# Optimization experiments

Measured on AMD Instinct MI355X. Metric: run time of the kernel, lower is better.

## Reference

```python
import jax, jax.numpy as jnp
import numpy as np

S, D, P, R, E, M, K = 1024, 1024, 2816, 64, 8, 16, 1


def setup_inputs() -> dict:
    key = jax.random.key(0)
    ks = jax.random.split(key, 10)
    xav_a = (2.0 / (P + R)) ** 0.5   # xavier_uniform-like std for adapters
    xav_d = (2.0 / (D + P)) ** 0.5   # xavier for down projections
    bank_s = (1.0 / D) ** 0.5        # keep basis columns O(1)
    return {
        "hidden_states": jax.random.normal(ks[0], (S, D), jnp.float32),
        "expert_indices": jax.random.randint(ks[1], (S, K), 0, E),
        "expert_weights": jax.random.uniform(ks[2], (S, K), jnp.float32),
        "up_adapters": jax.random.normal(ks[3], (E, P, R), jnp.float32) * xav_a,
        "gate_adapters": jax.random.normal(ks[4], (E, P, R), jnp.float32) * xav_a,
        "up_mixture_logits": jax.random.normal(ks[5], (E, M), jnp.float32) * 0.01,
        "gate_mixture_logits": jax.random.normal(ks[6], (E, M), jnp.float32) * 0.01,
        "down_projections": jax.random.normal(ks[7], (E, D, P), jnp.float32) * xav_d,
        "up_bank": jax.random.normal(ks[8], (M, D, R), jnp.float32) * bank_s,
        "gate_bank": jax.random.normal(ks[9], (M, D, R), jnp.float32) * bank_s,
    }


def reference(hidden_states, expert_indices, expert_weights,
              up_adapters, gate_adapters, up_mixture_logits,
              gate_mixture_logits, down_projections, up_bank, gate_bank):
    n_experts = down_projections.shape[0]
    # SparseMixer: token-independent mixture weights over global bases (softmax)
    alpha_up = jax.nn.softmax(up_mixture_logits, axis=-1)      # [E, M]
    alpha_gate = jax.nn.softmax(gate_mixture_logits, axis=-1)  # [E, M]
    # Compose per-expert mixed bases: sum_j alpha_{e,j} B_j -> [E, D, R]
    up_mixed = jnp.einsum('em,mdr->edr', alpha_up, up_bank)
    gate_mixed = jnp.einsum('em,mdr->edr', alpha_gate, gate_bank)
    # Recomposed Up/Gate weights: A_e @ mixed_e^T -> [E, P, D]
    W_up = jnp.einsum('epr,edr->epd', up_adapters, up_mixed)
    W_gate = jnp.einsum('epr,edr->epd', gate_adapters, gate_mixed)
    # Combine routing weights per (token, expert): sum over topk slots
    onehot = (expert_indices[..., None] == jnp.arange(n_experts)).astype(hidden_states.dtype)  # [S,K,E]
    comb = jnp.einsum('ske,sk->se', onehot, expert_weights)  # [S, E]
    out = jnp.zeros_like(hidden_states)
    for e in range(n_experts):  # fixed small expert count
        up = hidden_states @ W_up[e].T        # [S, P]
        gate = hidden_states @ W_gate[e].T    # [S, P]
        inter = jax.nn.silu(gate) * up        # gated activation
        out = out + (inter @ down_projections[e].T) * comb[:, e:e + 1]
    return out
```

## Files before the change

kernel.cpp:

```cpp
#include <hip/hip_runtime.h>
#include <hip/hip_bf16.h>
#include <math.h>

#define S 1024
#define D 1024
#define P 2816
#define R 64
#define E 8
#define M 16
#define KSPLIT 4
#define KQ (P / KSPLIT)
#define NIT (KQ / 64)
#define ZT 8
#define ACH ((E * P * R) / 8)

typedef __attribute__((ext_vector_type(8))) short short8;
typedef __attribute__((ext_vector_type(4))) float floatx4;

static __device__ inline unsigned short f2bf(float f) {
  __hip_bfloat16 h = __float2bfloat16(f);
  return *reinterpret_cast<unsigned short*>(&h);
}
static __device__ inline short8 pack8(float4 a, float4 b) {
  short8 v;
  v[0] = f2bf(a.x); v[1] = f2bf(a.y); v[2] = f2bf(a.z); v[3] = f2bf(a.w);
  v[4] = f2bf(b.x); v[5] = f2bf(b.y); v[6] = f2bf(b.z); v[7] = f2bf(b.w);
  return v;
}

__global__ __launch_bounds__(256) void k_pre(
    const float* __restrict__ up_logits, const float* __restrict__ gate_logits,
    const float* __restrict__ up_bank, const float* __restrict__ gate_bank,
    const float* __restrict__ H, const float* __restrict__ Aup,
    const float* __restrict__ Agate, const int* __restrict__ idx,
    unsigned short* __restrict__ Hbf, unsigned short* __restrict__ mxT,
    unsigned short* __restrict__ Aubf, unsigned short* __restrict__ Agbf,
    int* __restrict__ perm, int* __restrict__ offs) {
  int b = blockIdx.x, t = threadIdx.x;
  int g = b * 256 + t;

  if (b == 0) {
    __shared__ int hist[E];
    __shared__ int basearr[E];
    if (t < E) hist[t] = 0;
    __syncthreads();
    int e4[4];
#pragma unroll
    for (int j = 0; j < 4; ++j) {
      e4[j] = idx[t + j * 256];
      atomicAdd(&hist[e4[j]], 1);
    }
    __syncthreads();
    if (t == 0) {
      int run = 0;
      for (int i = 0; i < E; ++i) { basearr[i] = run; offs[i] = run; run += hist[i]; }
      offs[E] = S;
    }
    __syncthreads();
#pragma unroll
    for (int j = 0; j < 4; ++j) {
      int pos = atomicAdd(&basearr[e4[j]], 1);
      perm[pos] = t + j * 256;
    }
  }

  {
    const float* hs = H + (size_t)g * 16;
    float4 h0 = *(const float4*)hs, h1 = *(const float4*)(hs + 4);
    float4 h2 = *(const float4*)(hs + 8), h3 = *(const float4*)(hs + 12);
    *(short8*)(Hbf + (size_t)g * 16) = pack8(h0, h1);
    *(short8*)(Hbf + (size_t)g * 16 + 8) = pack8(h2, h3);
  }
#pragma unroll
  for (int j = 0; j < 3; ++j) {
    int c = g + j * 65536;
    if (c < ACH) {
      const float* su = Aup + (size_t)c * 8;
      const float* sg = Agate + (size_t)c * 8;
      float4 u0 = *(const float4*)su, u1 = *(const float4*)(su + 4);
      float4 g0 = *(const float4*)sg, g1 = *(const float4*)(sg + 4);
      *(short8*)(Aubf + (size_t)c * 8) = pack8(u0, u1);
      *(short8*)(Agbf + (size_t)c * 8) = pack8(g0, g1);
    }
  }

  __shared__ float alpha[2][E][M];
  if (t < 16) {
    int mat = t >> 3, e = t & 7;
    const float* lg = (mat ? gate_logits : up_logits) + e * M;
    float v[M], mx = -1e30f, s = 0.f;
#pragma unroll
    for (int m = 0; m < M; ++m) { v[m] = lg[m]; mx = fmaxf(mx, v[m]); }
#pragma unroll
    for (int m = 0; m < M; ++m) { v[m] = expf(v[m] - mx); s += v[m]; }
#pragma unroll
    for (int m = 0; m < M; ++m) alpha[mat][e][m] = v[m] / s;
  }
  __syncthreads();
  int d = g >> 6, r = g & 63;
  float au[E] = {0, 0, 0, 0, 0, 0, 0, 0}, ag[E] = {0, 0, 0, 0, 0, 0, 0, 0};
#pragma unroll
  for (int m = 0; m < M; ++m) {
    float vu = up_bank[((size_t)m * D + d) * R + r];
    float vg = gate_bank[((size_t)m * D + d) * R + r];
#pragma unroll
    for (int e = 0; e < E; ++e) {
      au[e] += alpha[0][e][m] * vu;
      ag[e] += alpha[1][e][m] * vg;
    }
  }
#pragma unroll
  for (int e = 0; e < E; ++e) {
    mxT[((size_t)e * 128 + r) * D + d] = f2bf(au[e]);
    mxT[((size_t)e * 128 + 64 + r) * D + d] = f2bf(ag[e]);
  }
}

__global__ __launch_bounds__(64) void k_t(
    const unsigned short* __restrict__ Hbf, const unsigned short* __restrict__ mxT,
    const int* __restrict__ perm, const int* __restrict__ offs,
    float* __restrict__ tpart) {
  int e = blockIdx.x;
  int end = offs[e + 1];
  int row0 = offs[e] + blockIdx.y * 16;
  if (row0 >= end) return;
  int lane = threadIdx.x & 63;
  int quad = lane >> 4, l15 = lane & 15;
  int z = blockIdx.z;
  int k0 = z * (D / ZT);
  int pos = row0 + l15;
  int tok = (pos < end) ? perm[pos] : -1;
  const unsigned short* hrow = Hbf + (size_t)(tok < 0 ? 0 : tok) * D + k0;
  const unsigned short* brow = mxT + (size_t)e * 128 * D + k0;
  floatx4 acc[8];
#pragma unroll
  for (int nt = 0; nt < 8; ++nt) acc[nt] = (floatx4){0.f, 0.f, 0.f, 0.f};
#pragma unroll
  for (int ks = 0; ks < 4; ++ks) {
    int kc = ks * 32 + quad * 8;
    short8 a = (short8){0, 0, 0, 0, 0, 0, 0, 0};
    if (tok >= 0) a = *(const short8*)(hrow + kc);
#pragma unroll
    for (int nt = 0; nt < 8; ++nt) {
      short8 bb = *(const short8*)(brow + (size_t)(nt * 16 + l15) * D + kc);
      acc[nt] = __builtin_amdgcn_mfma_f32_16x16x32_bf16(a, bb, acc[nt], 0, 0, 0);
    }
  }
#pragma unroll
  for (int reg = 0; reg < 4; ++reg) {
    int p = row0 + quad * 4 + reg;
    if (p < end) {
#pragma unroll
      for (int nt = 0; nt < 8; ++nt)
        tpart[((size_t)z * S + p) * 128 + nt * 16 + l15] = acc[nt][reg];
    }
  }
}

__global__ __launch_bounds__(256) void k_tred(
    const float* __restrict__ tpart, unsigned short* __restrict__ tbuf) {
  int i = (blockIdx.x * 256 + threadIdx.x) * 2;
  float2 s = make_float2(0.f, 0.f);
#pragma unroll
  for (int z = 0; z < ZT; ++z) {
    float2 v = *(const float2*)(tpart + (size_t)z * S * 128 + i);
    s.x += v.x; s.y += v.y;
  }
  unsigned int pk = (unsigned int)f2bf(s.x) | ((unsigned int)f2bf(s.y) << 16);
  *(unsigned int*)(tbuf + i) = pk;
}

__global__ __launch_bounds__(256) void k_inter(
    const unsigned short* __restrict__ tbuf, const unsigned short* __restrict__ Aubf,
    const unsigned short* __restrict__ Agbf, const int* __restrict__ offs,
    unsigned short* __restrict__ inter) {
  int e = blockIdx.x;
  int start = offs[e] + blockIdx.y * 16;
  int end = offs[e + 1];
  if (start >= end) return;
  int t = threadIdx.x, lane = t & 63, w = t >> 6;
  int quad = lane >> 4, l15 = lane & 15;
  int p0 = blockIdx.z * 256 + w * 64;
  int pos = start + l15;
  bool okA = pos < end;
  floatx4 accu[4], accg[4];
#pragma unroll
  for (int nt = 0; nt < 4; ++nt) {
    accu[nt] = (floatx4){0.f, 0.f, 0.f, 0.f};
    accg[nt] = (floatx4){0.f, 0.f, 0.f, 0.f};
  }
#pragma unroll
  for (int ks = 0; ks < 2; ++ks) {
    int kc = ks * 32 + quad * 8;
    short8 au = (short8){0, 0, 0, 0, 0, 0, 0, 0};
    short8 ag = (short8){0, 0, 0, 0, 0, 0, 0, 0};
    if (okA) {
      au = *(const short8*)(tbuf + (size_t)pos * 128 + kc);
      ag = *(const short8*)(tbuf + (size_t)pos * 128 + 64 + kc);
    }
#pragma unroll
    for (int nt = 0; nt < 4; ++nt) {
      size_t prow = (size_t)e * P + p0 + nt * 16 + l15;
      short8 bu = *(const short8*)(Aubf + prow * R + kc);
      short8 bg = *(const short8*)(Agbf + prow * R + kc);
      accu[nt] = __builtin_amdgcn_mfma_f32_16x16x32_bf16(au, bu, accu[nt], 0, 0, 0);
      accg[nt] = __builtin_amdgcn_mfma_f32_16x16x32_bf16(ag, bg, accg[nt], 0, 0, 0);
    }
  }
#pragma unroll
  for (int nt = 0; nt < 4; ++nt)
#pragma unroll
    for (int reg = 0; reg < 4; ++reg) {
      int prow = start + quad * 4 + reg;
      if (prow < end) {
        float gv = accg[nt][reg], uv = accu[nt][reg];
        float val = uv * (gv / (1.f + __expf(-gv)));
        inter[(size_t)prow * P + p0 + nt * 16 + l15] = f2bf(val);
      }
    }
}

__global__ __launch_bounds__(256) void k_down(
    const unsigned short* __restrict__ inter, const float* __restrict__ Wd,
    const int* __restrict__ offs, float* __restrict__ dpart) {
  int e = blockIdx.x;
  int start = offs[e];
  int end = offs[e + 1];
  if (start >= end) return;
  int kz = blockIdx.y;
  int d0 = blockIdx.z * 64;
  __shared__ unsigned short As[256][72];
  __shared__ unsigned short Bs[64][72];
  int t = threadIdx.x;
  int lane = t & 63, w = t >> 6, quad = lane >> 4, l15 = lane & 15;

  const unsigned short* aptr[8];
  bool aok[8];
#pragma unroll
  for (int j = 0; j < 8; ++j) {
    int arow = (t >> 3) + 32 * j;
    int pos = start + arow;
    aok[j] = (pos < end);
    aptr[j] = inter + (size_t)(aok[j] ? pos : start) * P + kz * KQ + (t & 7) * 8;
  }
  const float* bsrc = Wd + ((size_t)(e * D + d0 + (t >> 2)) * P + kz * KQ + (t & 3) * 16);

  float4 pa[8];
  float4 pb[4];
#pragma unroll
  for (int j = 0; j < 8; ++j)
    pa[j] = aok[j] ? *(const float4*)(aptr[j]) : make_float4(0.f, 0.f, 0.f, 0.f);
#pragma unroll
  for (int q = 0; q < 4; ++q) pb[q] = *(const float4*)(bsrc + q * 4);

  floatx4 acc[4][4];
#pragma unroll
  for (int tt = 0; tt < 4; ++tt)
#pragma unroll
    for (int dt = 0; dt < 4; ++dt) acc[tt][dt] = (floatx4){0.f, 0.f, 0.f, 0.f};

  for (int it = 0; it < NIT; ++it) {
#pragma unroll
    for (int j = 0; j < 8; ++j)
      *(float4*)&As[(t >> 3) + 32 * j][(t & 7) * 8] = pa[j];
    {
      short8 bv0, bv1;
      bv0[0] = f2bf(pb[0].x); bv0[1] = f2bf(pb[0].y); bv0[2] = f2bf(pb[0].z); bv0[3] = f2bf(pb[0].w);
      bv0[4] = f2bf(pb[1].x); bv0[5] = f2bf(pb[1].y); bv0[6] = f2bf(pb[1].z); bv0[7] = f2bf(pb[1].w);
      bv1[0] = f2bf(pb[2].x); bv1[1] = f2bf(pb[2].y); bv1[2] = f2bf(pb[2].z); bv1[3] = f2bf(pb[2].w);
      bv1[4] = f2bf(pb[3].x); bv1[5] = f2bf(pb[3].y); bv1[6] = f2bf(pb[3].z); bv1[7] = f2bf(pb[3].w);
      *(short8*)&Bs[t >> 2][(t & 3) * 16] = bv0;
      *(short8*)&Bs[t >> 2][(t & 3) * 16 + 8] = bv1;
    }
    __syncthreads();
    if (it + 1 < NIT) {
      int k0 = (it + 1) * 64;
#pragma unroll
      for (int j = 0; j < 8; ++j)
        pa[j] = aok[j] ? *(const float4*)(aptr[j] + k0) : make_float4(0.f, 0.f, 0.f, 0.f);
#pragma unroll
      for (int q = 0; q < 4; ++q) pb[q] = *(const float4*)(bsrc + k0 + q * 4);
    }
#pragma unroll
    for (int ks = 0; ks < 2; ++ks) {
      int kc = ks * 32 + quad * 8;
      short8 a[4], b[4];
#pragma unroll
      for (int tt = 0; tt < 4; ++tt) a[tt] = *(const short8*)&As[w * 64 + tt * 16 + l15][kc];
#pragma unroll
      for (int dt = 0; dt < 4; ++dt) b[dt] = *(const short8*)&Bs[dt * 16 + l15][kc];
#pragma unroll
      for (int tt = 0; tt < 4; ++tt)
#pragma unroll
        for (int dt = 0; dt < 4; ++dt)
          acc[tt][dt] = __builtin_amdgcn_mfma_f32_16x16x32_bf16(a[tt], b[dt], acc[tt][dt], 0, 0, 0);
    }
    __syncthreads();
  }
  float* dp = dpart + (size_t)kz * S * D;
#pragma unroll
  for (int tt = 0; tt < 4; ++tt)
#pragma unroll
    for (int reg = 0; reg < 4; ++reg) {
      int pos = start + w * 64 + tt * 16 + quad * 4 + reg;
      if (pos < end) {
#pragma unroll
        for (int dt = 0; dt < 4; ++dt)
          dp[(size_t)pos * D + d0 + dt * 16 + l15] = acc[tt][dt][reg];
      }
    }
}

__global__ __launch_bounds__(256) void k_red(
    const float* __restrict__ dpart, const int* __restrict__ perm,
    const float* __restrict__ wts, float* __restrict__ out) {
  int t = threadIdx.x;
  int row = blockIdx.x * 4 + (t >> 6);
  int lane = t & 63;
  int tok = perm[row];
  float wt = wts[tok];
  const float* src = dpart + (size_t)row * D + lane * 4;
  float* dst = out + (size_t)tok * D + lane * 4;
#pragma unroll
  for (int j = 0; j < 4; ++j) {
    float4 s = *(const float4*)(src + j * 256);
#pragma unroll
    for (int kz = 1; kz < KSPLIT; ++kz) {
      float4 v = *(const float4*)(src + (size_t)kz * S * D + j * 256);
      s.x += v.x; s.y += v.y; s.z += v.z; s.w += v.w;
    }
    s.x *= wt; s.y *= wt; s.z *= wt; s.w *= wt;
    *(float4*)(dst + j * 256) = s;
  }
}

extern "C" void kernel_launch(void* const* d_in, const int* in_sizes, int n_in,
                              void* d_out, int out_size, void* d_ws, size_t ws_size,
                              hipStream_t stream) {
  const float* H = (const float*)d_in[0];
  const int* idx = (const int*)d_in[1];
  const float* wts = (const float*)d_in[2];
  const float* Aup = (const float*)d_in[3];
  const float* Agate = (const float*)d_in[4];
  const float* upl = (const float*)d_in[5];
  const float* gatel = (const float*)d_in[6];
  const float* Wd = (const float*)d_in[7];
  const float* upb = (const float*)d_in[8];
  const float* gateb = (const float*)d_in[9];
  float* out = (float*)d_out;

  char* ws = (char*)d_ws;
  unsigned short* Hbf = (unsigned short*)ws;
  unsigned short* mxT = Hbf + (size_t)S * D;
  unsigned short* Aubf = mxT + (size_t)E * 128 * D;
  unsigned short* Agbf = Aubf + (size_t)E * P * R;
  unsigned short* inter = Agbf + (size_t)E * P * R;
  unsigned short* tbuf = inter + (size_t)S * P;
  float* tpart = (float*)(tbuf + (size_t)S * 128);
  float* dpart = tpart + (size_t)ZT * S * 128;
  int* perm = (int*)(dpart + (size_t)KSPLIT * S * D);
  int* offs = perm + S;

  k_pre<<<256, 256, 0, stream>>>(upl, gatel, upb, gateb, H, Aup, Agate, idx,
                                 Hbf, mxT, Aubf, Agbf, perm, offs);
  k_t<<<dim3(E, 16, ZT), 64, 0, stream>>>(Hbf, mxT, perm, offs, tpart);
  k_tred<<<256, 256, 0, stream>>>(tpart, tbuf);
  k_inter<<<dim3(E, 16, P / 256), 256, 0, stream>>>(tbuf, Aubf, Agbf, offs, inter);
  k_down<<<dim3(E, KSPLIT, D / 64), 256, 0, stream>>>(inter, Wd, offs, dpart);
  k_red<<<256, 256, 0, stream>>>(dpart, perm, wts, out);
}
```

Before: 217.6 us.

## Split basis mixing into tiled kernel with coalesced transposed stores; double k_t split-K

The softmax-weighted basis mixing moves out of k_pre into a new k_mix kernel. It reads the banks as float4, transposes through an LDS tile, and writes mxT in contiguous 16-element bf16 chunks instead of scattered 2-byte stores strided by D. Separately, the k_t split-K factor goes from 8 to 16 with half the inner k-steps, giving more blocks for the small token-by-basis GEMM. The cost is one extra kernel launch and a larger partial buffer for k_tred to reduce.

```diff
diff --git a/kernel.cpp b/kernel.cpp
--- a/kernel.cpp
+++ b/kernel.cpp
@@ -11,7 +11,7 @@
 #define KSPLIT 4
 #define KQ (P / KSPLIT)
 #define NIT (KQ / 64)
-#define ZT 8
+#define ZT 16
 #define ACH ((E * P * R) / 8)
 
 typedef __attribute__((ext_vector_type(8))) short short8;
@@ -29,13 +29,11 @@
 }
 
 __global__ __launch_bounds__(256) void k_pre(
-    const float* __restrict__ up_logits, const float* __restrict__ gate_logits,
-    const float* __restrict__ up_bank, const float* __restrict__ gate_bank,
     const float* __restrict__ H, const float* __restrict__ Aup,
     const float* __restrict__ Agate, const int* __restrict__ idx,
-    unsigned short* __restrict__ Hbf, unsigned short* __restrict__ mxT,
-    unsigned short* __restrict__ Aubf, unsigned short* __restrict__ Agbf,
-    int* __restrict__ perm, int* __restrict__ offs) {
+    unsigned short* __restrict__ Hbf, unsigned short* __restrict__ Aubf,
+    unsigned short* __restrict__ Agbf, int* __restrict__ perm,
+    int* __restrict__ offs) {
   int b = blockIdx.x, t = threadIdx.x;
   int g = b * 256 + t;
 
@@ -83,36 +81,63 @@
       *(short8*)(Agbf + (size_t)c * 8) = pack8(g0, g1);
     }
   }
-
-  __shared__ float alpha[2][E][M];
-  if (t < 16) {
-    int mat = t >> 3, e = t & 7;
-    const float* lg = (mat ? gate_logits : up_logits) + e * M;
+}
+
+__global__ __launch_bounds__(256) void k_mix(
+    const float* __restrict__ up_logits, const float* __restrict__ gate_logits,
+    const float* __restrict__ up_bank, const float* __restrict__ gate_bank,
+    unsigned short* __restrict__ mxT) {
+  int mat = blockIdx.x;
+  int d0 = blockIdx.y * 16;
+  const float* bank = mat ? gate_bank : up_bank;
+  __shared__ float alpha[E][M];
+  __shared__ float tile[E][64][17];
+  int t = threadIdx.x;
+  if (t < E) {
+    const float* lg = (mat ? gate_logits : up_logits) + t * M;
     float v[M], mx = -1e30f, s = 0.f;
 #pragma unroll
     for (int m = 0; m < M; ++m) { v[m] = lg[m]; mx = fmaxf(mx, v[m]); }
 #pragma unroll
     for (int m = 0; m < M; ++m) { v[m] = expf(v[m] - mx); s += v[m]; }
 #pragma unroll
-    for (int m = 0; m < M; ++m) alpha[mat][e][m] = v[m] / s;
+    for (int m = 0; m < M; ++m) alpha[t][m] = v[m] / s;
   }
   __syncthreads();
-  int d = g >> 6, r = g & 63;
-  float au[E] = {0, 0, 0, 0, 0, 0, 0, 0}, ag[E] = {0, 0, 0, 0, 0, 0, 0, 0};
-#pragma unroll
+  int r4 = (t & 15) * 4;
+  int dg = t >> 4;
+  float val[E][4];
+#pragma unroll
+  for (int e = 0; e < E; ++e)
+#pragma unroll
+    for (int i = 0; i < 4; ++i) val[e][i] = 0.f;
   for (int m = 0; m < M; ++m) {
-    float vu = up_bank[((size_t)m * D + d) * R + r];
-    float vg = gate_bank[((size_t)m * D + d) * R + r];
+    float4 bv = *(const float4*)(bank + ((size_t)m * D + d0 + dg) * R + r4);
 #pragma unroll
     for (int e = 0; e < E; ++e) {
-      au[e] += alpha[0][e][m] * vu;
-      ag[e] += alpha[1][e][m] * vg;
-    }
-  }
-#pragma unroll
-  for (int e = 0; e < E; ++e) {
-    mxT[((size_t)e * 128 + r) * D + d] = f2bf(au[e]);
-    mxT[((size_t)e * 128 + 64 + r) * D + d] = f2bf(ag[e]);
+      float a = alpha[e][m];
+      val[e][0] += a * bv.x; val[e][1] += a * bv.y;
+      val[e][2] += a * bv.z; val[e][3] += a * bv.w;
+    }
+  }
+#pragma unroll
+  for (int e = 0; e < E; ++e)
+#pragma unroll
+    for (int i = 0; i < 4; ++i) tile[e][r4 + i][dg] = val[e][i];
+  __syncthreads();
+  int e = t >> 5;
+#pragma unroll
+  for (int half = 0; half < 2; ++half) {
+    int rr = (t & 31) + half * 32;
+    short8 o0, o1;
+#pragma unroll
+    for (int j = 0; j < 8; ++j) {
+      o0[j] = (short)f2bf(tile[e][rr][j]);
+      o1[j] = (short)f2bf(tile[e][rr][8 + j]);
+    }
+    unsigned short* dst = mxT + ((size_t)(e * 128 + mat * 64 + rr)) * D + d0;
+    *(short8*)dst = o0;
+    *(short8*)(dst + 8) = o1;
   }
 }
 
@@ -136,7 +161,7 @@
 #pragma unroll
   for (int nt = 0; nt < 8; ++nt) acc[nt] = (floatx4){0.f, 0.f, 0.f, 0.f};
 #pragma unroll
-  for (int ks = 0; ks < 4; ++ks) {
+  for (int ks = 0; ks < 2; ++ks) {
     int kc = ks * 32 + quad * 8;
     short8 a = (short8){0, 0, 0, 0, 0, 0, 0, 0};
     if (tok >= 0) a = *(const short8*)(hrow + kc);
@@ -361,8 +386,8 @@
   int* perm = (int*)(dpart + (size_t)KSPLIT * S * D);
   int* offs = perm + S;
 
-  k_pre<<<256, 256, 0, stream>>>(upl, gatel, upb, gateb, H, Aup, Agate, idx,
-                                 Hbf, mxT, Aubf, Agbf, perm, offs);
+  k_pre<<<256, 256, 0, stream>>>(H, Aup, Agate, idx, Hbf, Aubf, Agbf, perm, offs);
+  k_mix<<<dim3(2, D / 16), 256, 0, stream>>>(upl, gatel, upb, gateb, mxT);
   k_t<<<dim3(E, 16, ZT), 64, 0, stream>>>(Hbf, mxT, perm, offs, tpart);
   k_tred<<<256, 256, 0, stream>>>(tpart, tbuf);
   k_inter<<<dim3(E, 16, P / 256), 256, 0, stream>>>(tbuf, Aubf, Agbf, offs, inter);
```

New measurement: 214.9 us. About the same (-1.2%).
